# Performance work log

Hardware: AMD Instinct MI355X
Metric: run time of the kernel (lower is better)

## Reference

```python
import jax, jax.numpy as jnp
import numpy as np

INF = 1e30
B, L, D_IN, D_STATE, HIDDEN = 32, 4096, 150, 75, 75


def setup_inputs() -> dict:
    key = jax.random.key(0)
    k_in, k_st, k_m, k_w0, k_b0, k_w1, k_b1 = jax.random.split(key, 7)
    inputs = jax.random.normal(k_in, (B, L, D_IN), dtype=jnp.float32)
    state = jax.random.normal(k_st, (B, D_STATE), dtype=jnp.float32)
    c_mask = jax.random.randint(k_m, (B, L), 0, 2).astype(bool)
    # Linear params; torch nn.Linear init scale ~ 1/sqrt(fan_in)
    W0 = jax.random.normal(k_w0, (D_STATE + D_IN, HIDDEN), dtype=jnp.float32) / np.sqrt(D_STATE + D_IN)
    b0 = jax.random.normal(k_b0, (HIDDEN,), dtype=jnp.float32) / np.sqrt(D_STATE + D_IN)
    W1 = jax.random.normal(k_w1, (HIDDEN, 1), dtype=jnp.float32) / np.sqrt(HIDDEN)
    b1 = jax.random.normal(k_b1, (1,), dtype=jnp.float32) / np.sqrt(HIDDEN)
    return {"inputs": inputs, "state": state, "c_mask": c_mask,
            "W0": W0, "b0": b0, "W1": W1, "b1": b1}


def reference(inputs, state, c_mask, W0, b0, W1, b1):
    b, l, _ = inputs.shape
    # u: [B, L, D_STATE + D_IN]  (state broadcast along L, concat with inputs)
    u = jnp.concatenate(
        [jnp.broadcast_to(state[:, None, :], (b, l, state.shape[-1])), inputs],
        axis=2)
    s0 = jnp.tanh(u @ W0 + b0)               # [B, L, HIDDEN]
    s = (s0 @ W1 + b1)[..., 0]               # [B, L]
    s1 = s - INF * (1.0 - c_mask.astype(s.dtype))
    a = jax.nn.softmax(s1, axis=-1)           # [B, L]
    res = jnp.sum(inputs * a[..., None], axis=1, keepdims=True)  # [B, 1, D_IN]
    return res, s1
```

## Files before the change

kernel.cpp:

```cpp
#include <hip/hip_runtime.h>

#define B_    32
#define L_    4096
#define DIN   150
#define DST   75
#define HID   75
#define INF30 1e30f


__global__ void k_zero(float* __restrict__ p, int n) {
    int i = blockIdx.x * 256 + threadIdx.x;
    if (i < n) p[i] = 0.f;
}

__global__ __launch_bounds__(128) void k_statepre(
    const float* __restrict__ state, const float* __restrict__ W0,
    const float* __restrict__ b0, float* __restrict__ sp) {
    int b = blockIdx.x;
    int h = threadIdx.x;
    if (h < HID) {
        float acc = b0[h];
        #pragma unroll 5
        for (int k = 0; k < DST; ++k)
            acc = fmaf(state[b * DST + k], W0[k * HID + h], acc);
        sp[b * HID + h] = acc;
    }
}

#define ROWS 64
#define CW   50
#define CPAD 51
__global__ __launch_bounds__(64) void k_score(
    const float* __restrict__ in, const unsigned char* __restrict__ maskB,
    const float* __restrict__ W0, const float* __restrict__ W1,
    const float* __restrict__ b1, const float* __restrict__ sp,
    float* __restrict__ s1out) {
    __shared__ float xs[ROWS * CPAD];
    int blk = blockIdx.x;
    int b   = blk >> 6;
    int l0  = (blk & 63) * ROWS;
    int tid = threadIdx.x;

    const float* src = in + (size_t)(b * L_ + l0) * DIN;

    float pre[HID];
    #pragma unroll
    for (int h = 0; h < HID; ++h) pre[h] = sp[b * HID + h];

    const float* w0i = W0 + DST * HID;

    for (int c = 0; c < 3; ++c) {
        __syncthreads();
        for (int i = tid; i < ROWS * CW; i += 64) {
            int r = i / CW;
            int d = i - r * CW;
            xs[r * CPAD + d] = src[r * DIN + c * CW + d];
        }
        __syncthreads();
        #pragma unroll 2
        for (int d = 0; d < CW; ++d) {
            float x = xs[tid * CPAD + d];
            const float* wr = w0i + (c * CW + d) * HID;
            #pragma unroll
            for (int h = 0; h < HID; ++h) pre[h] = fmaf(x, wr[h], pre[h]);
        }
    }

    float s = b1[0];
    #pragma unroll
    for (int h = 0; h < HID; ++h) {
        float p  = pre[h];
        float e  = __expf(-2.f * fabsf(p));
        float th = (1.f - e) / (1.f + e);
        s = fmaf(copysignf(th, p), W1[h], s);
    }

    unsigned char probe = maskB[tid * 4 + 1];
    bool isI32 = __all(probe == 0);
    int l = l0 + tid;
    bool mv;
    if (isI32) mv = ((const int*)maskB)[b * L_ + l] != 0;
    else       mv = maskB[b * L_ + l] != 0;
    s1out[b * L_ + l] = s - (mv ? 0.f : INF30);
}

__global__ __launch_bounds__(256) void k_stats(
    const float* __restrict__ s1, float* __restrict__ mOut,
    float* __restrict__ invOut) {
    int b = blockIdx.x;
    int tid = threadIdx.x;
    const float* row = s1 + b * L_;

    float m = -INFINITY;
    for (int i = tid; i < L_; i += 256) m = fmaxf(m, row[i]);
    #pragma unroll
    for (int off = 32; off; off >>= 1) m = fmaxf(m, __shfl_down(m, off, 64));
    __shared__ float red[4];
    if ((tid & 63) == 0) red[tid >> 6] = m;
    __syncthreads();
    m = fmaxf(fmaxf(red[0], red[1]), fmaxf(red[2], red[3]));

    float sum = 0.f;
    for (int i = tid; i < L_; i += 256) sum += __expf(row[i] - m);
    #pragma unroll
    for (int off = 32; off; off >>= 1) sum += __shfl_down(sum, off, 64);
    __shared__ float red2[4];
    if ((tid & 63) == 0) red2[tid >> 6] = sum;
    __syncthreads();
    if (tid == 0) {
        mOut[b]   = m;
        invOut[b] = 1.f / (red2[0] + red2[1] + red2[2] + red2[3]);
    }
}

#define CHUNK 128
__global__ __launch_bounds__(192) void k_weighted(
    const float* __restrict__ in, const float* __restrict__ s1,
    const float* __restrict__ mIn, const float* __restrict__ invIn,
    float* __restrict__ res) {
    int b   = blockIdx.y;
    int l0  = blockIdx.x * CHUNK;
    int tid = threadIdx.x;
    __shared__ float w[CHUNK];
    float m = mIn[b], inv = invIn[b];
    if (tid < CHUNK)
        w[tid] = __expf(s1[b * L_ + l0 + tid] - m) * inv;
    __syncthreads();
    if (tid < DIN) {
        float acc = 0.f;
        const float* p = in + (size_t)(b * L_ + l0) * DIN + tid;
        #pragma unroll 4
        for (int i = 0; i < CHUNK; ++i) acc = fmaf(w[i], p[i * DIN], acc);
        atomicAdd(&res[b * DIN + tid], acc);
    }
}

extern "C" void kernel_launch(void* const* d_in, const int* in_sizes, int n_in,
                              void* d_out, int out_size, void* d_ws, size_t ws_size,
                              hipStream_t stream) {
    const float*         inputs = (const float*)d_in[0];
    const float*         state  = (const float*)d_in[1];
    const unsigned char* cmask  = (const unsigned char*)d_in[2];
    const float*         W0     = (const float*)d_in[3];
    const float*         b0     = (const float*)d_in[4];
    const float*         W1     = (const float*)d_in[5];
    const float*         b1     = (const float*)d_in[6];

    float* res   = (float*)d_out;
    float* s1    = (float*)d_out + B_ * DIN;
    float* wsf   = (float*)d_ws;
    float* sp    = wsf;
    float* mBuf  = wsf + B_ * HID;
    float* invB  = wsf + B_ * HID + B_;

    k_zero<<<(B_ * DIN + 255) / 256, 256, 0, stream>>>(res, B_ * DIN);
    k_statepre<<<B_, 128, 0, stream>>>(state, W0, b0, sp);
    k_score<<<B_ * L_ / ROWS, ROWS, 0, stream>>>(inputs, cmask, W0, W1, b1, sp, s1);
    k_stats<<<B_, 256, 0, stream>>>(s1, mBuf, invB);
    dim3 gridW(L_ / CHUNK, B_);
    k_weighted<<<gridW, 192, 0, stream>>>(inputs, s1, mBuf, invB, res);
}
```

Before: 226.0 us.

## Split hidden units across four waves in score kernel and widen reductions

The score kernel now uses 256 threads per 64-row tile. Each wave computes 20 of the hidden units, padded to 80, and the four partial scores are reduced through shared memory. This cuts per-thread register pressure from a 75-float accumulator and raises occupancy, and a new prep kernel pads W0 and W1 to aligned rows. The stats kernel moves to 1024 threads and the weighted-sum chunk is halved to 64 with deeper unroll, adding parallelism at the cost of more atomics and an extra launch.

Result: slower. 324.7 us (+43.7%).

```diff
diff --git a/kernel.cpp b/kernel.cpp
--- a/kernel.cpp
+++ b/kernel.cpp
@@ -5,6 +5,7 @@
 #define DIN   150
 #define DST   75
 #define HID   75
+#define HPAD  80
 #define INF30 1e30f
 
 
@@ -13,107 +14,138 @@
     if (i < n) p[i] = 0.f;
 }
 
+__global__ __launch_bounds__(256) void k_prep(
+    const float* __restrict__ W0, const float* __restrict__ W1,
+    float* __restrict__ W0p, float* __restrict__ W1p) {
+    int i = blockIdx.x * 256 + threadIdx.x;
+    if (i < DIN * HPAD) {
+        int d = i / HPAD, h = i - d * HPAD;
+        W0p[i] = (h < HID) ? W0[(DST + d) * HID + h] : 0.f;
+    }
+    if (i < HPAD) W1p[i] = (i < HID) ? W1[i] : 0.f;
+}
+
 __global__ __launch_bounds__(128) void k_statepre(
     const float* __restrict__ state, const float* __restrict__ W0,
     const float* __restrict__ b0, float* __restrict__ sp) {
     int b = blockIdx.x;
     int h = threadIdx.x;
-    if (h < HID) {
-        float acc = b0[h];
-        #pragma unroll 5
-        for (int k = 0; k < DST; ++k)
-            acc = fmaf(state[b * DST + k], W0[k * HID + h], acc);
-        sp[b * HID + h] = acc;
+    if (h < HPAD) {
+        float acc = 0.f;
+        if (h < HID) {
+            acc = b0[h];
+            #pragma unroll 5
+            for (int k = 0; k < DST; ++k)
+                acc = fmaf(state[b * DST + k], W0[k * HID + h], acc);
+        }
+        sp[b * HPAD + h] = acc;
     }
 }
 
-#define ROWS 64
-#define CW   50
-#define CPAD 51
-__global__ __launch_bounds__(64) void k_score(
+#define CW2  75
+#define XPAD 77
+__global__ __launch_bounds__(256, 8) void k_score(
     const float* __restrict__ in, const unsigned char* __restrict__ maskB,
-    const float* __restrict__ W0, const float* __restrict__ W1,
+    const float* __restrict__ W0p, const float* __restrict__ W1p,
     const float* __restrict__ b1, const float* __restrict__ sp,
     float* __restrict__ s1out) {
-    __shared__ float xs[ROWS * CPAD];
-    int blk = blockIdx.x;
-    int b   = blk >> 6;
-    int l0  = (blk & 63) * ROWS;
-    int tid = threadIdx.x;
+    __shared__ float xs[64 * XPAD];
+    int blk  = blockIdx.x;
+    int b    = blk >> 6;
+    int l0   = (blk & 63) * 64;
+    int tid  = threadIdx.x;
+    int w    = tid >> 6;
+    int lane = tid & 63;
+    int hlo  = w * 20;
 
     const float* src = in + (size_t)(b * L_ + l0) * DIN;
 
-    float pre[HID];
+    float pre[20];
     #pragma unroll
-    for (int h = 0; h < HID; ++h) pre[h] = sp[b * HID + h];
+    for (int h = 0; h < 20; ++h) pre[h] = sp[b * HPAD + hlo + h];
 
-    const float* w0i = W0 + DST * HID;
-
-    for (int c = 0; c < 3; ++c) {
+    for (int c = 0; c < 2; ++c) {
         __syncthreads();
-        for (int i = tid; i < ROWS * CW; i += 64) {
-            int r = i / CW;
-            int d = i - r * CW;
-            xs[r * CPAD + d] = src[r * DIN + c * CW + d];
+        for (int i = tid; i < 64 * CW2; i += 256) {
+            int r = i / CW2;
+            int d = i - r * CW2;
+            xs[r * XPAD + d] = src[r * DIN + c * CW2 + d];
         }
         __syncthreads();
-        #pragma unroll 2
-        for (int d = 0; d < CW; ++d) {
-            float x = xs[tid * CPAD + d];
-            const float* wr = w0i + (c * CW + d) * HID;
+        #pragma unroll 3
+        for (int dj = 0; dj < CW2; ++dj) {
+            float x = xs[lane * XPAD + dj];
+            const float* wr = W0p + (c * CW2 + dj) * HPAD + hlo;
             #pragma unroll
-            for (int h = 0; h < HID; ++h) pre[h] = fmaf(x, wr[h], pre[h]);
+            for (int h = 0; h < 20; ++h) pre[h] = fmaf(x, wr[h], pre[h]);
         }
     }
 
-    float s = b1[0];
+    float sw = 0.f;
     #pragma unroll
-    for (int h = 0; h < HID; ++h) {
+    for (int h = 0; h < 20; ++h) {
         float p  = pre[h];
         float e  = __expf(-2.f * fabsf(p));
         float th = (1.f - e) / (1.f + e);
-        s = fmaf(copysignf(th, p), W1[h], s);
+        sw = fmaf(copysignf(th, p), W1p[hlo + h], sw);
     }
 
-    unsigned char probe = maskB[tid * 4 + 1];
-    bool isI32 = __all(probe == 0);
-    int l = l0 + tid;
-    bool mv;
-    if (isI32) mv = ((const int*)maskB)[b * L_ + l] != 0;
-    else       mv = maskB[b * L_ + l] != 0;
-    s1out[b * L_ + l] = s - (mv ? 0.f : INF30);
+    __syncthreads();
+    xs[w * 64 + lane] = sw;
+    __syncthreads();
+
+    if (w == 0) {
+        float s = xs[lane] + xs[64 + lane] + xs[128 + lane] + xs[192 + lane]
+                + b1[0];
+        unsigned char probe = maskB[lane * 4 + 1];
+        bool isI32 = __all(probe == 0);
+        int l = l0 + lane;
+        bool mv = isI32 ? (((const int*)maskB)[b * L_ + l] != 0)
+                        : (maskB[b * L_ + l] != 0);
+        s1out[b * L_ + l] = s - (mv ? 0.f : INF30);
+    }
 }
 
-__global__ __launch_bounds__(256) void k_stats(
+__global__ __launch_bounds__(1024) void k_stats(
     const float* __restrict__ s1, float* __restrict__ mOut,
     float* __restrict__ invOut) {
     int b = blockIdx.x;
     int tid = threadIdx.x;
+    int wid = tid >> 6;
     const float* row = s1 + b * L_;
+    __shared__ float red[16];
+    __shared__ float mfin;
 
     float m = -INFINITY;
-    for (int i = tid; i < L_; i += 256) m = fmaxf(m, row[i]);
+    for (int i = tid; i < L_; i += 1024) m = fmaxf(m, row[i]);
     #pragma unroll
     for (int off = 32; off; off >>= 1) m = fmaxf(m, __shfl_down(m, off, 64));
-    __shared__ float red[4];
-    if ((tid & 63) == 0) red[tid >> 6] = m;
+    if ((tid & 63) == 0) red[wid] = m;
     __syncthreads();
-    m = fmaxf(fmaxf(red[0], red[1]), fmaxf(red[2], red[3]));
+    if (tid == 0) {
+        float mm = red[0];
+        for (int j = 1; j < 16; ++j) mm = fmaxf(mm, red[j]);
+        mfin = mm;
+    }
+    __syncthreads();
+    m = mfin;
 
     float sum = 0.f;
-    for (int i = tid; i < L_; i += 256) sum += __expf(row[i] - m);
+    for (int i = tid; i < L_; i += 1024) sum += __expf(row[i] - m);
     #pragma unroll
     for (int off = 32; off; off >>= 1) sum += __shfl_down(sum, off, 64);
-    __shared__ float red2[4];
-    if ((tid & 63) == 0) red2[tid >> 6] = sum;
+    __syncthreads();
+    if ((tid & 63) == 0) red[wid] = sum;
     __syncthreads();
     if (tid == 0) {
+        float ss = 0.f;
+        for (int j = 0; j < 16; ++j) ss += red[j];
         mOut[b]   = m;
-        invOut[b] = 1.f / (red2[0] + red2[1] + red2[2] + red2[3]);
+        invOut[b] = 1.f / ss;
     }
 }
 
-#define CHUNK 128
+#define CHUNK 64
 __global__ __launch_bounds__(192) void k_weighted(
     const float* __restrict__ in, const float* __restrict__ s1,
     const float* __restrict__ mIn, const float* __restrict__ invIn,
@@ -129,7 +161,7 @@
     if (tid < DIN) {
         float acc = 0.f;
         const float* p = in + (size_t)(b * L_ + l0) * DIN + tid;
-        #pragma unroll 4
+        #pragma unroll 8
         for (int i = 0; i < CHUNK; ++i) acc = fmaf(w[i], p[i * DIN], acc);
         atomicAdd(&res[b * DIN + tid], acc);
     }
@@ -149,14 +181,17 @@
     float* res   = (float*)d_out;
     float* s1    = (float*)d_out + B_ * DIN;
     float* wsf   = (float*)d_ws;
-    float* sp    = wsf;
-    float* mBuf  = wsf + B_ * HID;
-    float* invB  = wsf + B_ * HID + B_;
+    float* W0p   = wsf;
+    float* W1p   = W0p + DIN * HPAD;
+    float* sp    = W1p + HPAD;
+    float* mBuf  = sp + B_ * HPAD;
+    float* invB  = mBuf + B_;
 
     k_zero<<<(B_ * DIN + 255) / 256, 256, 0, stream>>>(res, B_ * DIN);
+    k_prep<<<(DIN * HPAD + 255) / 256, 256, 0, stream>>>(W0, W1, W0p, W1p);
     k_statepre<<<B_, 128, 0, stream>>>(state, W0, b0, sp);
-    k_score<<<B_ * L_ / ROWS, ROWS, 0, stream>>>(inputs, cmask, W0, W1, b1, sp, s1);
-    k_stats<<<B_, 256, 0, stream>>>(s1, mBuf, invB);
+    k_score<<<B_ * L_ / 64, 256, 0, stream>>>(inputs, cmask, W0p, W1p, b1, sp, s1);
+    k_stats<<<B_, 1024, 0, stream>>>(s1, mBuf, invB);
     dim3 gridW(L_ / CHUNK, B_);
     k_weighted<<<gridW, 192, 0, stream>>>(inputs, s1, mBuf, invB, res);
 }
```
